# Kernel optimization log

Hardware: AMD Instinct MI355X
Metric: run time of the kernel (lower is better)

Reference implementation:

```python
import jax, jax.numpy as jnp
import numpy as np

N = 100000      # nodes
E = 1600000     # directed edges (avg degree 16)
D_IN, D_H, D_OUT = 128, 128, 64


def glorot(k, fi, fo):
    s = (6.0 / (fi + fo)) ** 0.5
    return jax.random.uniform(k, (fi, fo), jnp.float32, -s, s)


def setup_inputs() -> dict:
    key = jax.random.key(0)
    ks = jax.random.split(key, 5)
    edges = jax.random.randint(ks[0], (2, E), 0, N)
    features = jax.random.normal(ks[1], (N, D_IN), dtype=jnp.float32)
    return dict(
        edges=edges,
        features=features,
        W0=glorot(ks[2], D_IN, D_H), b0=jnp.zeros((D_H,), jnp.float32),
        W1=glorot(ks[3], D_H, D_H), b1=jnp.zeros((D_H,), jnp.float32),
        W2=glorot(ks[4], D_H, D_OUT), b2=jnp.zeros((D_OUT,), jnp.float32),
    )


def _prep(edges):
    # add self-loops and compute symmetric GCN normalization D^-1/2 A_hat D^-1/2
    loop = jnp.arange(N)
    row = jnp.concatenate([edges[0], loop])  # source
    col = jnp.concatenate([edges[1], loop])  # target
    deg = jax.ops.segment_sum(jnp.ones((row.shape[0],), jnp.float32), col, num_segments=N)
    dinv = jnp.where(deg > 0, jax.lax.rsqrt(deg), 0.0)
    norm = dinv[row] * dinv[col]             # per-edge coefficient
    return row, col, norm


def gcn_conv(x, row, col, norm, W, b):
    x = x @ W                                 # [N, out]
    msg = x[row] * norm[:, None]              # gather + scale, [E+N, out]
    return jax.ops.segment_sum(msg, col, num_segments=N) + b


def reference(edges, features, W0, b0, W1, b1, W2, b2):
    row, col, norm = _prep(edges)
    h = jax.nn.relu(gcn_conv(features, row, col, norm, W0, b0))
    h = jax.nn.relu(gcn_conv(h, row, col, norm, W1, b1))
    h = gcn_conv(h, row, col, norm, W2, b2)
    return jax.nn.log_softmax(h, axis=1)
```

## Files before the change

### kernel.cpp

```cpp
#include <hip/hip_runtime.h>
#include <hip/hip_bf16.h>
#include <math.h>

#define NN 100000
#define EE 1600000
#define NB2 391
#define NPART 256
#define STAGE 4864

typedef __attribute__((ext_vector_type(8))) short short8;
typedef __attribute__((ext_vector_type(4))) float f32x4;

__device__ inline unsigned short f2bf(float x) {
    unsigned u = __float_as_uint(x);
    unsigned r = u + 0x7FFFu + ((u >> 16) & 1u);
    return (unsigned short)(r >> 16);
}
__device__ inline unsigned pack2bf(float a, float b) {
    return (unsigned)f2bf(a) | ((unsigned)f2bf(b) << 16);
}
__device__ inline float bflo(unsigned u) { return __uint_as_float(u << 16); }
__device__ inline float bfhi(unsigned u) { return __uint_as_float(u & 0xFFFF0000u); }


__global__ __launch_bounds__(256) void part_hist(const int* __restrict__ dst,
                                                 int* __restrict__ hist, int e) {
    __shared__ int h[NB2];
    for (int i = threadIdx.x; i < NB2; i += 256) h[i] = 0;
    __syncthreads();
    int chunk = (e + NPART - 1) / NPART;
    int b0 = blockIdx.x * chunk, b1 = min(e, b0 + chunk);
    for (int i = b0 + threadIdx.x; i < b1; i += 256)
        atomicAdd(&h[dst[i] >> 8], 1);
    __syncthreads();
    for (int i = threadIdx.x; i < NB2; i += 256)
        hist[i * NPART + blockIdx.x] = h[i];
}

__global__ void scan_block_plain(int* __restrict__ a, int* __restrict__ bsum, int n) {
    __shared__ int s[256];
    int t = threadIdx.x;
    int g = blockIdx.x * 256 + t;
    int v = (g < n) ? a[g] : 0;
    s[t] = v;
    for (int d = 1; d < 256; d <<= 1) {
        __syncthreads();
        int x = (t >= d) ? s[t - d] : 0;
        __syncthreads();
        s[t] += x;
    }
    if (g < n) a[g] = s[t] - v;
    if (t == 255) bsum[blockIdx.x] = s[255];
}

__global__ void scan_sums(int* __restrict__ bsum, int nb) {
    __shared__ int s[512];
    int t = threadIdx.x;
    int v = (t < nb) ? bsum[t] : 0;
    s[t] = v;
    for (int d = 1; d < 512; d <<= 1) {
        __syncthreads();
        int x = (t >= d) ? s[t - d] : 0;
        __syncthreads();
        s[t] += x;
    }
    if (t < nb) bsum[t] = s[t] - v;
}

__global__ void scan_add_plain(int* __restrict__ a, const int* __restrict__ bsum, int n) {
    int g = blockIdx.x * 256 + threadIdx.x;
    if (g < n) a[g] += bsum[blockIdx.x];
}

__global__ __launch_bounds__(256) void part_scatter(const int* __restrict__ src,
                                                    const int* __restrict__ dst,
                                                    const int* __restrict__ hist,
                                                    int2* __restrict__ P, int e) {
    __shared__ int cur[NB2];
    for (int i = threadIdx.x; i < NB2; i += 256) cur[i] = hist[i * NPART + blockIdx.x];
    __syncthreads();
    int chunk = (e + NPART - 1) / NPART;
    int b0 = blockIdx.x * chunk, b1 = min(e, b0 + chunk);
    for (int i = b0 + threadIdx.x; i < b1; i += 256) {
        int d = dst[i];
        int p = atomicAdd(&cur[d >> 8], 1);
        P[p] = make_int2(src[i], d);
    }
}

__global__ __launch_bounds__(256) void bucket_count(const int2* __restrict__ P,
                                                    const int* __restrict__ hist,
                                                    int* __restrict__ offs,
                                                    float* __restrict__ dinv, int e, int n) {
    __shared__ int cnt[256];
    __shared__ int s[256];
    int b = blockIdx.x;
    int t = threadIdx.x;
    int base = hist[b * NPART];
    int end = (b == NB2 - 1) ? e : hist[(b + 1) * NPART];
    cnt[t] = 0;
    __syncthreads();
    for (int i = base + t; i < end; i += 256)
        atomicAdd(&cnt[P[i].y & 255], 1);
    __syncthreads();
    int v = cnt[t];
    s[t] = v;
    for (int d = 1; d < 256; d <<= 1) {
        __syncthreads();
        int x = (t >= d) ? s[t - d] : 0;
        __syncthreads();
        s[t] += x;
    }
    int node = b * 256 + t;
    if (node < n) {
        offs[node] = base + s[t] - v;
        dinv[node] = 1.0f / sqrtf((float)(v + 1));
    }
    if (b == NB2 - 1 && t == 0) offs[n] = e;
}

__global__ __launch_bounds__(256) void bucket_scatter(const int2* __restrict__ P,
                                                      const int* __restrict__ hist,
                                                      const int* __restrict__ offs,
                                                      const float* __restrict__ dinv,
                                                      int2* __restrict__ csr2, int e, int n) {
    __shared__ int cur[256];
    __shared__ int2 stage[STAGE];
    int b = blockIdx.x;
    int t = threadIdx.x;
    int base = hist[b * NPART];
    int end = (b == NB2 - 1) ? e : hist[(b + 1) * NPART];
    int node = b * 256 + t;
    cur[t] = (node < n) ? (offs[node] - base) : 0;
    __syncthreads();
    for (int i = base + t; i < end; i += 256) {
        int2 sd = P[i];
        int p = atomicAdd(&cur[sd.y & 255], 1);
        int2 entry = make_int2(sd.x, __float_as_int(dinv[sd.x]));
        if (p < STAGE) stage[p] = entry;
        else csr2[base + p] = entry;
    }
    __syncthreads();
    int m = end - base;
    if (m > STAGE) m = STAGE;
    for (int i = t; i < m; i += 256) csr2[base + i] = stage[i];
}


__global__ void prep_weights(const float* __restrict__ W0, const float* __restrict__ W1,
                             const float* __restrict__ W2, unsigned short* __restrict__ Wt0,
                             unsigned short* __restrict__ Wt1, unsigned short* __restrict__ Wt2) {
    int g = blockIdx.x * 256 + threadIdx.x;
    if (g < 16384) {
        int n = g >> 7, k = g & 127;
        Wt0[g] = f2bf(W0[k * 128 + n]);
    } else if (g < 32768) {
        int i = g - 16384;
        int n = i >> 7, k = i & 127;
        Wt1[i] = f2bf(W1[k * 128 + n]);
    } else if (g < 40960) {
        int i = g - 32768;
        int n = i >> 7, k = i & 127;
        Wt2[i] = f2bf(W2[k * 64 + n]);
    }
}

template <int DOUT, bool A_IS_F32>
__global__ __launch_bounds__(256) void gemm_mfma(const void* __restrict__ Aptr,
                                                 const unsigned short* __restrict__ Wt,
                                                 unsigned short* __restrict__ Y, int nrows) {
    constexpr int KP = 136;
    constexpr int NT = DOUT / 16;
    __shared__ unsigned short sA[128 * KP];
    __shared__ unsigned short sB[DOUT * KP];
    const int row0 = blockIdx.x * 128;
    const int tid = threadIdx.x;

    for (int i = tid; i < DOUT * 16; i += 256) {
        int n = i >> 4, c = (i & 15) * 8;
        uint4 v = *(const uint4*)(Wt + n * 128 + c);
        *(uint4*)(&sB[n * KP + c]) = v;
    }
    if (A_IS_F32) {
        const float* A = (const float*)Aptr;
        for (int i = tid; i < 128 * 32; i += 256) {
            int r = i >> 5, c = (i & 31) * 4;
            float4 v = make_float4(0.f, 0.f, 0.f, 0.f);
            if (row0 + r < nrows) v = *(const float4*)(A + (size_t)(row0 + r) * 128 + c);
            uint2 o;
            o.x = pack2bf(v.x, v.y);
            o.y = pack2bf(v.z, v.w);
            *(uint2*)(&sA[r * KP + c]) = o;
        }
    } else {
        const unsigned short* A = (const unsigned short*)Aptr;
        for (int i = tid; i < 128 * 16; i += 256) {
            int r = i >> 4, c = (i & 15) * 8;
            uint4 v = make_uint4(0u, 0u, 0u, 0u);
            if (row0 + r < nrows) v = *(const uint4*)(A + (size_t)(row0 + r) * 128 + c);
            *(uint4*)(&sA[r * KP + c]) = v;
        }
    }
    __syncthreads();

    const int wave = tid >> 6;
    const int lane = tid & 63;
    const int m0 = lane & 15;
    const int kq = (lane >> 4) * 8;

    f32x4 acc[2][NT];
#pragma unroll
    for (int rt = 0; rt < 2; ++rt)
#pragma unroll
        for (int t = 0; t < NT; ++t) acc[rt][t] = (f32x4){0.f, 0.f, 0.f, 0.f};

#pragma unroll
    for (int k0 = 0; k0 < 128; k0 += 32) {
        short8 a0 = *(const short8*)(&sA[(wave * 32 + m0) * KP + k0 + kq]);
        short8 a1 = *(const short8*)(&sA[(wave * 32 + 16 + m0) * KP + k0 + kq]);
#pragma unroll
        for (int t = 0; t < NT; ++t) {
            short8 b = *(const short8*)(&sB[(t * 16 + m0) * KP + k0 + kq]);
            acc[0][t] = __builtin_amdgcn_mfma_f32_16x16x32_bf16(a0, b, acc[0][t], 0, 0, 0);
            acc[1][t] = __builtin_amdgcn_mfma_f32_16x16x32_bf16(a1, b, acc[1][t], 0, 0, 0);
        }
    }

#pragma unroll
    for (int rt = 0; rt < 2; ++rt)
#pragma unroll
        for (int t = 0; t < NT; ++t)
#pragma unroll
            for (int r = 0; r < 4; ++r) {
                int row = row0 + wave * 32 + rt * 16 + (lane >> 4) * 4 + r;
                if (row < nrows)
                    Y[(size_t)row * DOUT + t * 16 + (lane & 15)] = f2bf(acc[rt][t][r]);
            }
}

__global__ __launch_bounds__(256) void agg128_bf16(const unsigned short* __restrict__ Xp,
                                                   const int2* __restrict__ csr2,
                                                   const int* __restrict__ offs,
                                                   const float* __restrict__ dinv,
                                                   const float* __restrict__ bias,
                                                   unsigned short* __restrict__ Y, int n) {
    int node = blockIdx.x * 4 + (threadIdx.x >> 6);
    if (node >= n) return;
    int lane = threadIdx.x & 63;
    int q = lane >> 4;
    int l = lane & 15;
    float di = dinv[node];
    int s = offs[node], e = offs[node + 1];
    float a0 = 0.f, a1 = 0.f, a2 = 0.f, a3 = 0.f, a4 = 0.f, a5 = 0.f, a6 = 0.f, a7 = 0.f;
    int p = s + q;
    for (; p + 4 < e; p += 8) {
        int2 sv0 = csr2[p];
        int2 sv1 = csr2[p + 4];
        float c0 = __int_as_float(sv0.y) * di;
        float c1 = __int_as_float(sv1.y) * di;
        uint4 u0 = *(const uint4*)(Xp + (size_t)sv0.x * 128 + l * 8);
        uint4 u1 = *(const uint4*)(Xp + (size_t)sv1.x * 128 + l * 8);
        a0 = fmaf(c0, bflo(u0.x), a0); a1 = fmaf(c0, bfhi(u0.x), a1);
        a2 = fmaf(c0, bflo(u0.y), a2); a3 = fmaf(c0, bfhi(u0.y), a3);
        a4 = fmaf(c0, bflo(u0.z), a4); a5 = fmaf(c0, bfhi(u0.z), a5);
        a6 = fmaf(c0, bflo(u0.w), a6); a7 = fmaf(c0, bfhi(u0.w), a7);
        a0 = fmaf(c1, bflo(u1.x), a0); a1 = fmaf(c1, bfhi(u1.x), a1);
        a2 = fmaf(c1, bflo(u1.y), a2); a3 = fmaf(c1, bfhi(u1.y), a3);
        a4 = fmaf(c1, bflo(u1.z), a4); a5 = fmaf(c1, bfhi(u1.z), a5);
        a6 = fmaf(c1, bflo(u1.w), a6); a7 = fmaf(c1, bfhi(u1.w), a7);
    }
    if (p < e) {
        int2 sv = csr2[p];
        float c = __int_as_float(sv.y) * di;
        uint4 u = *(const uint4*)(Xp + (size_t)sv.x * 128 + l * 8);
        a0 = fmaf(c, bflo(u.x), a0); a1 = fmaf(c, bfhi(u.x), a1);
        a2 = fmaf(c, bflo(u.y), a2); a3 = fmaf(c, bfhi(u.y), a3);
        a4 = fmaf(c, bflo(u.z), a4); a5 = fmaf(c, bfhi(u.z), a5);
        a6 = fmaf(c, bflo(u.w), a6); a7 = fmaf(c, bfhi(u.w), a7);
    }
    if (q == 0) {
        float cs = di * di;
        uint4 u = *(const uint4*)(Xp + (size_t)node * 128 + l * 8);
        a0 = fmaf(cs, bflo(u.x), a0); a1 = fmaf(cs, bfhi(u.x), a1);
        a2 = fmaf(cs, bflo(u.y), a2); a3 = fmaf(cs, bfhi(u.y), a3);
        a4 = fmaf(cs, bflo(u.z), a4); a5 = fmaf(cs, bfhi(u.z), a5);
        a6 = fmaf(cs, bflo(u.w), a6); a7 = fmaf(cs, bfhi(u.w), a7);
    }
    a0 += __shfl_xor(a0, 16); a0 += __shfl_xor(a0, 32);
    a1 += __shfl_xor(a1, 16); a1 += __shfl_xor(a1, 32);
    a2 += __shfl_xor(a2, 16); a2 += __shfl_xor(a2, 32);
    a3 += __shfl_xor(a3, 16); a3 += __shfl_xor(a3, 32);
    a4 += __shfl_xor(a4, 16); a4 += __shfl_xor(a4, 32);
    a5 += __shfl_xor(a5, 16); a5 += __shfl_xor(a5, 32);
    a6 += __shfl_xor(a6, 16); a6 += __shfl_xor(a6, 32);
    a7 += __shfl_xor(a7, 16); a7 += __shfl_xor(a7, 32);
    if (q == 0) {
        float4 bA = *(const float4*)(bias + l * 8);
        float4 bB = *(const float4*)(bias + l * 8 + 4);
        a0 = fmaxf(a0 + bA.x, 0.f); a1 = fmaxf(a1 + bA.y, 0.f);
        a2 = fmaxf(a2 + bA.z, 0.f); a3 = fmaxf(a3 + bA.w, 0.f);
        a4 = fmaxf(a4 + bB.x, 0.f); a5 = fmaxf(a5 + bB.y, 0.f);
        a6 = fmaxf(a6 + bB.z, 0.f); a7 = fmaxf(a7 + bB.w, 0.f);
        uint4 o;
        o.x = pack2bf(a0, a1); o.y = pack2bf(a2, a3);
        o.z = pack2bf(a4, a5); o.w = pack2bf(a6, a7);
        *(uint4*)(Y + (size_t)node * 128 + l * 8) = o;
    }
}

__global__ __launch_bounds__(256) void agg_softmax64_bf16(const unsigned short* __restrict__ Xp,
                                                          const int2* __restrict__ csr2,
                                                          const int* __restrict__ offs,
                                                          const float* __restrict__ dinv,
                                                          const float* __restrict__ bias,
                                                          float* __restrict__ out, int n) {
    int node = blockIdx.x * 4 + (threadIdx.x >> 6);
    if (node >= n) return;
    int lane = threadIdx.x & 63;
    int g8 = lane >> 3;
    int l = lane & 7;
    float di = dinv[node];
    int s = offs[node], e = offs[node + 1];
    float a0 = 0.f, a1 = 0.f, a2 = 0.f, a3 = 0.f, a4 = 0.f, a5 = 0.f, a6 = 0.f, a7 = 0.f;
    int p = s + g8;
    for (; p + 8 < e; p += 16) {
        int2 sv0 = csr2[p];
        int2 sv1 = csr2[p + 8];
        float c0 = __int_as_float(sv0.y) * di;
        float c1 = __int_as_float(sv1.y) * di;
        uint4 u0 = *(const uint4*)(Xp + (size_t)sv0.x * 64 + l * 8);
        uint4 u1 = *(const uint4*)(Xp + (size_t)sv1.x * 64 + l * 8);
        a0 = fmaf(c0, bflo(u0.x), a0); a1 = fmaf(c0, bfhi(u0.x), a1);
        a2 = fmaf(c0, bflo(u0.y), a2); a3 = fmaf(c0, bfhi(u0.y), a3);
        a4 = fmaf(c0, bflo(u0.z), a4); a5 = fmaf(c0, bfhi(u0.z), a5);
        a6 = fmaf(c0, bflo(u0.w), a6); a7 = fmaf(c0, bfhi(u0.w), a7);
        a0 = fmaf(c1, bflo(u1.x), a0); a1 = fmaf(c1, bfhi(u1.x), a1);
        a2 = fmaf(c1, bflo(u1.y), a2); a3 = fmaf(c1, bfhi(u1.y), a3);
        a4 = fmaf(c1, bflo(u1.z), a4); a5 = fmaf(c1, bfhi(u1.z), a5);
        a6 = fmaf(c1, bflo(u1.w), a6); a7 = fmaf(c1, bfhi(u1.w), a7);
    }
    if (p < e) {
        int2 sv = csr2[p];
        float c = __int_as_float(sv.y) * di;
        uint4 u = *(const uint4*)(Xp + (size_t)sv.x * 64 + l * 8);
        a0 = fmaf(c, bflo(u.x), a0); a1 = fmaf(c, bfhi(u.x), a1);
        a2 = fmaf(c, bflo(u.y), a2); a3 = fmaf(c, bfhi(u.y), a3);
        a4 = fmaf(c, bflo(u.z), a4); a5 = fmaf(c, bfhi(u.z), a5);
        a6 = fmaf(c, bflo(u.w), a6); a7 = fmaf(c, bfhi(u.w), a7);
    }
    if (g8 == 0) {
        float cs = di * di;
        uint4 u = *(const uint4*)(Xp + (size_t)node * 64 + l * 8);
        a0 = fmaf(cs, bflo(u.x), a0); a1 = fmaf(cs, bfhi(u.x), a1);
        a2 = fmaf(cs, bflo(u.y), a2); a3 = fmaf(cs, bfhi(u.y), a3);
        a4 = fmaf(cs, bflo(u.z), a4); a5 = fmaf(cs, bfhi(u.z), a5);
        a6 = fmaf(cs, bflo(u.w), a6); a7 = fmaf(cs, bfhi(u.w), a7);
    }
    a0 += __shfl_xor(a0, 8); a0 += __shfl_xor(a0, 16); a0 += __shfl_xor(a0, 32);
    a1 += __shfl_xor(a1, 8); a1 += __shfl_xor(a1, 16); a1 += __shfl_xor(a1, 32);
    a2 += __shfl_xor(a2, 8); a2 += __shfl_xor(a2, 16); a2 += __shfl_xor(a2, 32);
    a3 += __shfl_xor(a3, 8); a3 += __shfl_xor(a3, 16); a3 += __shfl_xor(a3, 32);
    a4 += __shfl_xor(a4, 8); a4 += __shfl_xor(a4, 16); a4 += __shfl_xor(a4, 32);
    a5 += __shfl_xor(a5, 8); a5 += __shfl_xor(a5, 16); a5 += __shfl_xor(a5, 32);
    a6 += __shfl_xor(a6, 8); a6 += __shfl_xor(a6, 16); a6 += __shfl_xor(a6, 32);
    a7 += __shfl_xor(a7, 8); a7 += __shfl_xor(a7, 16); a7 += __shfl_xor(a7, 32);
    if (g8 == 0) {
        float4 bA = *(const float4*)(bias + l * 8);
        float4 bB = *(const float4*)(bias + l * 8 + 4);
        a0 += bA.x; a1 += bA.y; a2 += bA.z; a3 += bA.w;
        a4 += bB.x; a5 += bB.y; a6 += bB.z; a7 += bB.w;
        float m = fmaxf(fmaxf(fmaxf(a0, a1), fmaxf(a2, a3)), fmaxf(fmaxf(a4, a5), fmaxf(a6, a7)));
#pragma unroll
        for (int o = 4; o > 0; o >>= 1) m = fmaxf(m, __shfl_xor(m, o));
        float ssum = __expf(a0 - m) + __expf(a1 - m) + __expf(a2 - m) + __expf(a3 - m) +
                     __expf(a4 - m) + __expf(a5 - m) + __expf(a6 - m) + __expf(a7 - m);
#pragma unroll
        for (int o = 4; o > 0; o >>= 1) ssum += __shfl_xor(ssum, o);
        float lg = m + __logf(ssum);
        float4 r0 = make_float4(a0 - lg, a1 - lg, a2 - lg, a3 - lg);
        float4 r1 = make_float4(a4 - lg, a5 - lg, a6 - lg, a7 - lg);
        *(float4*)(out + (size_t)node * 64 + l * 8) = r0;
        *(float4*)(out + (size_t)node * 64 + l * 8 + 4) = r1;
    }
}


extern "C" void kernel_launch(void* const* d_in, const int* in_sizes, int n_in,
                              void* d_out, int out_size, void* d_ws, size_t ws_size,
                              hipStream_t stream) {
    const int* edges = (const int*)d_in[0];
    const float* feat = (const float*)d_in[1];
    const float* W0 = (const float*)d_in[2];
    const float* b0 = (const float*)d_in[3];
    const float* W1 = (const float*)d_in[4];
    const float* b1 = (const float*)d_in[5];
    const float* W2 = (const float*)d_in[6];
    const float* b2 = (const float*)d_in[7];

    const int N = NN;
    const int E = EE;
    const int HN = NB2 * NPART;
    const int HB = HN / 256;

    char* ws = (char*)d_ws;
    int* hist = (int*)ws;
    int* bsum = hist + HN;
    int* offs = bsum + 512;
    float* dinv = (float*)(offs + N + 1);
    size_t io = (size_t)((char*)(dinv + N) - ws);
    io = (io + 15) & ~(size_t)15;
    int2* P = (int2*)(ws + io);
    int2* csr2 = P + E;
    unsigned short* Wt0 = (unsigned short*)(csr2 + E);
    unsigned short* Wt1 = Wt0 + 16384;
    unsigned short* Wt2 = Wt1 + 16384;
    size_t off = (size_t)((char*)(Wt2 + 8192) - ws);
    off = (off + 255) & ~(size_t)255;
    unsigned short* bufA = (unsigned short*)(ws + off);
    unsigned short* bufB = bufA + (size_t)N * 128;

    const int* esrc = edges;
    const int* edst = edges + E;

    prep_weights<<<160, 256, 0, stream>>>(W0, W1, W2, Wt0, Wt1, Wt2);
    part_hist<<<NPART, 256, 0, stream>>>(edst, hist, E);
    scan_block_plain<<<HB, 256, 0, stream>>>(hist, bsum, HN);
    scan_sums<<<1, 512, 0, stream>>>(bsum, HB);
    scan_add_plain<<<HB, 256, 0, stream>>>(hist, bsum, HN);
    part_scatter<<<NPART, 256, 0, stream>>>(esrc, edst, hist, P, E);
    bucket_count<<<NB2, 256, 0, stream>>>(P, hist, offs, dinv, E, N);
    bucket_scatter<<<NB2, 256, 0, stream>>>(P, hist, offs, dinv, csr2, E, N);

    const int gemmBlocks = (N + 127) / 128;
    const int aggBlocks = (N + 3) / 4;

    gemm_mfma<128, true><<<gemmBlocks, 256, 0, stream>>>(feat, Wt0, bufA, N);
    agg128_bf16<<<aggBlocks, 256, 0, stream>>>(bufA, csr2, offs, dinv, b0, bufB, N);
    gemm_mfma<128, false><<<gemmBlocks, 256, 0, stream>>>(bufB, Wt1, bufA, N);
    agg128_bf16<<<aggBlocks, 256, 0, stream>>>(bufA, csr2, offs, dinv, b1, bufB, N);
    gemm_mfma<64, false><<<gemmBlocks, 256, 0, stream>>>(bufB, Wt2, bufA, N);
    agg_softmax64_bf16<<<aggBlocks, 256, 0, stream>>>(bufA, csr2, offs, dinv, b2, (float*)d_out, N);
}
```

Baseline: 419.2 us.

## Fold source-side normalization into GEMM epilogue and shrink CSR to plain indices

Each GEMM output row is now pre-scaled by dinv[row], so aggregation sums neighbor rows without per-edge coefficients and applies the destination dinv once at the end. The CSR entries drop from (src, dinv) int2 pairs to a single int, and partition entries pack src and the low destination bits into one int. The two bucket kernels merge into a single kernel. The 128-wide aggregation loop is unrolled to four outstanding gathers. These changes cut edge-stream bytes and per-edge multiplies in the memory-bound gather. The cost is one extra bf16 rounding of pre-scaled values, and the packing assumes src << 8 fits in 31 bits.

```diff
diff --git a/kernel.cpp b/kernel.cpp
--- a/kernel.cpp
+++ b/kernel.cpp
@@ -6,10 +6,11 @@
 #define EE 1600000
 #define NB2 391
 #define NPART 256
-#define STAGE 4864
+#define STAGE 6144
 
 typedef __attribute__((ext_vector_type(8))) short short8;
 typedef __attribute__((ext_vector_type(4))) float f32x4;
+typedef __attribute__((ext_vector_type(2))) float f32x2;
 
 __device__ inline unsigned short f2bf(float x) {
     unsigned u = __float_as_uint(x);
@@ -19,8 +20,12 @@
 __device__ inline unsigned pack2bf(float a, float b) {
     return (unsigned)f2bf(a) | ((unsigned)f2bf(b) << 16);
 }
-__device__ inline float bflo(unsigned u) { return __uint_as_float(u << 16); }
-__device__ inline float bfhi(unsigned u) { return __uint_as_float(u & 0xFFFF0000u); }
+__device__ inline f32x2 bf2f2(unsigned u) {
+    f32x2 r;
+    r.x = __uint_as_float(u << 16);
+    r.y = __uint_as_float(u & 0xFFFF0000u);
+    return r;
+}
 
 
 __global__ __launch_bounds__(256) void part_hist(const int* __restrict__ dst,
@@ -75,7 +80,7 @@
 __global__ __launch_bounds__(256) void part_scatter(const int* __restrict__ src,
                                                     const int* __restrict__ dst,
                                                     const int* __restrict__ hist,
-                                                    int2* __restrict__ P, int e) {
+                                                    int* __restrict__ P, int e) {
     __shared__ int cur[NB2];
     for (int i = threadIdx.x; i < NB2; i += 256) cur[i] = hist[i * NPART + blockIdx.x];
     __syncthreads();
@@ -84,66 +89,56 @@
     for (int i = b0 + threadIdx.x; i < b1; i += 256) {
         int d = dst[i];
         int p = atomicAdd(&cur[d >> 8], 1);
-        P[p] = make_int2(src[i], d);
-    }
-}
-
-__global__ __launch_bounds__(256) void bucket_count(const int2* __restrict__ P,
+        P[p] = (src[i] << 8) | (d & 255);
+    }
+}
+
+__global__ __launch_bounds__(256) void bucket_build(const int* __restrict__ P,
                                                     const int* __restrict__ hist,
                                                     int* __restrict__ offs,
-                                                    float* __restrict__ dinv, int e, int n) {
+                                                    float* __restrict__ dinv,
+                                                    int* __restrict__ csr, int e, int n) {
     __shared__ int cnt[256];
-    __shared__ int s[256];
-    int b = blockIdx.x;
-    int t = threadIdx.x;
+    __shared__ int sc[256];
+    __shared__ int cur[256];
+    __shared__ int stage[STAGE];
+    int b = blockIdx.x, t = threadIdx.x;
     int base = hist[b * NPART];
     int end = (b == NB2 - 1) ? e : hist[(b + 1) * NPART];
     cnt[t] = 0;
     __syncthreads();
     for (int i = base + t; i < end; i += 256)
-        atomicAdd(&cnt[P[i].y & 255], 1);
+        atomicAdd(&cnt[P[i] & 255], 1);
     __syncthreads();
     int v = cnt[t];
-    s[t] = v;
+    sc[t] = v;
     for (int d = 1; d < 256; d <<= 1) {
         __syncthreads();
-        int x = (t >= d) ? s[t - d] : 0;
-        __syncthreads();
-        s[t] += x;
-    }
+        int x = (t >= d) ? sc[t - d] : 0;
+        __syncthreads();
+        sc[t] += x;
+    }
+    __syncthreads();
+    int myoff = sc[t] - v;
     int node = b * 256 + t;
     if (node < n) {
-        offs[node] = base + s[t] - v;
+        offs[node] = base + myoff;
         dinv[node] = 1.0f / sqrtf((float)(v + 1));
     }
     if (b == NB2 - 1 && t == 0) offs[n] = e;
-}
-
-__global__ __launch_bounds__(256) void bucket_scatter(const int2* __restrict__ P,
-                                                      const int* __restrict__ hist,
-                                                      const int* __restrict__ offs,
-                                                      const float* __restrict__ dinv,
-                                                      int2* __restrict__ csr2, int e, int n) {
-    __shared__ int cur[256];
-    __shared__ int2 stage[STAGE];
-    int b = blockIdx.x;
-    int t = threadIdx.x;
-    int base = hist[b * NPART];
-    int end = (b == NB2 - 1) ? e : hist[(b + 1) * NPART];
-    int node = b * 256 + t;
-    cur[t] = (node < n) ? (offs[node] - base) : 0;
+    cur[t] = myoff;
     __syncthreads();
     for (int i = base + t; i < end; i += 256) {
-        int2 sd = P[i];
-        int p = atomicAdd(&cur[sd.y & 255], 1);
-        int2 entry = make_int2(sd.x, __float_as_int(dinv[sd.x]));
-        if (p < STAGE) stage[p] = entry;
-        else csr2[base + p] = entry;
+        int pe = P[i];
+        int p = atomicAdd(&cur[pe & 255], 1);
+        int sv = ((unsigned)pe) >> 8;
+        if (p < STAGE) stage[p] = sv;
+        else csr[base + p] = sv;
     }
     __syncthreads();
     int m = end - base;
     if (m > STAGE) m = STAGE;
-    for (int i = t; i < m; i += 256) csr2[base + i] = stage[i];
+    for (int i = t; i < m; i += 256) csr[base + i] = stage[i];
 }
 
 
@@ -168,6 +163,7 @@
 template <int DOUT, bool A_IS_F32>
 __global__ __launch_bounds__(256) void gemm_mfma(const void* __restrict__ Aptr,
                                                  const unsigned short* __restrict__ Wt,
+                                                 const float* __restrict__ dinv,
                                                  unsigned short* __restrict__ Y, int nrows) {
     constexpr int KP = 136;
     constexpr int NT = DOUT / 16;
@@ -229,17 +225,19 @@
 #pragma unroll
     for (int rt = 0; rt < 2; ++rt)
 #pragma unroll
-        for (int t = 0; t < NT; ++t)
-#pragma unroll
-            for (int r = 0; r < 4; ++r) {
-                int row = row0 + wave * 32 + rt * 16 + (lane >> 4) * 4 + r;
-                if (row < nrows)
-                    Y[(size_t)row * DOUT + t * 16 + (lane & 15)] = f2bf(acc[rt][t][r]);
+        for (int r = 0; r < 4; ++r) {
+            int row = row0 + wave * 32 + rt * 16 + (lane >> 4) * 4 + r;
+            if (row < nrows) {
+                float dv = dinv[row];
+#pragma unroll
+                for (int t = 0; t < NT; ++t)
+                    Y[(size_t)row * DOUT + t * 16 + (lane & 15)] = f2bf(acc[rt][t][r] * dv);
             }
+        }
 }
 
 __global__ __launch_bounds__(256) void agg128_bf16(const unsigned short* __restrict__ Xp,
-                                                   const int2* __restrict__ csr2,
+                                                   const int* __restrict__ csr,
                                                    const int* __restrict__ offs,
                                                    const float* __restrict__ dinv,
                                                    const float* __restrict__ bias,
@@ -249,67 +247,56 @@
     int lane = threadIdx.x & 63;
     int q = lane >> 4;
     int l = lane & 15;
-    float di = dinv[node];
     int s = offs[node], e = offs[node + 1];
-    float a0 = 0.f, a1 = 0.f, a2 = 0.f, a3 = 0.f, a4 = 0.f, a5 = 0.f, a6 = 0.f, a7 = 0.f;
+    f32x2 a0 = {0.f, 0.f}, a1 = {0.f, 0.f}, a2 = {0.f, 0.f}, a3 = {0.f, 0.f};
     int p = s + q;
-    for (; p + 4 < e; p += 8) {
-        int2 sv0 = csr2[p];
-        int2 sv1 = csr2[p + 4];
-        float c0 = __int_as_float(sv0.y) * di;
-        float c1 = __int_as_float(sv1.y) * di;
-        uint4 u0 = *(const uint4*)(Xp + (size_t)sv0.x * 128 + l * 8);
-        uint4 u1 = *(const uint4*)(Xp + (size_t)sv1.x * 128 + l * 8);
-        a0 = fmaf(c0, bflo(u0.x), a0); a1 = fmaf(c0, bfhi(u0.x), a1);
-        a2 = fmaf(c0, bflo(u0.y), a2); a3 = fmaf(c0, bfhi(u0.y), a3);
-        a4 = fmaf(c0, bflo(u0.z), a4); a5 = fmaf(c0, bfhi(u0.z), a5);
-        a6 = fmaf(c0, bflo(u0.w), a6); a7 = fmaf(c0, bfhi(u0.w), a7);
-        a0 = fmaf(c1, bflo(u1.x), a0); a1 = fmaf(c1, bfhi(u1.x), a1);
-        a2 = fmaf(c1, bflo(u1.y), a2); a3 = fmaf(c1, bfhi(u1.y), a3);
-        a4 = fmaf(c1, bflo(u1.z), a4); a5 = fmaf(c1, bfhi(u1.z), a5);
-        a6 = fmaf(c1, bflo(u1.w), a6); a7 = fmaf(c1, bfhi(u1.w), a7);
-    }
-    if (p < e) {
-        int2 sv = csr2[p];
-        float c = __int_as_float(sv.y) * di;
-        uint4 u = *(const uint4*)(Xp + (size_t)sv.x * 128 + l * 8);
-        a0 = fmaf(c, bflo(u.x), a0); a1 = fmaf(c, bfhi(u.x), a1);
-        a2 = fmaf(c, bflo(u.y), a2); a3 = fmaf(c, bfhi(u.y), a3);
-        a4 = fmaf(c, bflo(u.z), a4); a5 = fmaf(c, bfhi(u.z), a5);
-        a6 = fmaf(c, bflo(u.w), a6); a7 = fmaf(c, bfhi(u.w), a7);
+    for (; p + 12 < e; p += 16) {
+        int s0 = csr[p], s1 = csr[p + 4], s2 = csr[p + 8], s3 = csr[p + 12];
+        uint4 u0 = *(const uint4*)(Xp + (size_t)s0 * 128 + l * 8);
+        uint4 u1 = *(const uint4*)(Xp + (size_t)s1 * 128 + l * 8);
+        uint4 u2 = *(const uint4*)(Xp + (size_t)s2 * 128 + l * 8);
+        uint4 u3 = *(const uint4*)(Xp + (size_t)s3 * 128 + l * 8);
+        a0 += bf2f2(u0.x); a1 += bf2f2(u0.y); a2 += bf2f2(u0.z); a3 += bf2f2(u0.w);
+        a0 += bf2f2(u1.x); a1 += bf2f2(u1.y); a2 += bf2f2(u1.z); a3 += bf2f2(u1.w);
+        a0 += bf2f2(u2.x); a1 += bf2f2(u2.y); a2 += bf2f2(u2.z); a3 += bf2f2(u2.w);
+        a0 += bf2f2(u3.x); a1 += bf2f2(u3.y); a2 += bf2f2(u3.z); a3 += bf2f2(u3.w);
+    }
+    for (; p < e; p += 4) {
+        int s0 = csr[p];
+        uint4 u = *(const uint4*)(Xp + (size_t)s0 * 128 + l * 8);
+        a0 += bf2f2(u.x); a1 += bf2f2(u.y); a2 += bf2f2(u.z); a3 += bf2f2(u.w);
     }
     if (q == 0) {
-        float cs = di * di;
         uint4 u = *(const uint4*)(Xp + (size_t)node * 128 + l * 8);
-        a0 = fmaf(cs, bflo(u.x), a0); a1 = fmaf(cs, bfhi(u.x), a1);
-        a2 = fmaf(cs, bflo(u.y), a2); a3 = fmaf(cs, bfhi(u.y), a3);
-        a4 = fmaf(cs, bflo(u.z), a4); a5 = fmaf(cs, bfhi(u.z), a5);
-        a6 = fmaf(cs, bflo(u.w), a6); a7 = fmaf(cs, bfhi(u.w), a7);
-    }
-    a0 += __shfl_xor(a0, 16); a0 += __shfl_xor(a0, 32);
-    a1 += __shfl_xor(a1, 16); a1 += __shfl_xor(a1, 32);
-    a2 += __shfl_xor(a2, 16); a2 += __shfl_xor(a2, 32);
-    a3 += __shfl_xor(a3, 16); a3 += __shfl_xor(a3, 32);
-    a4 += __shfl_xor(a4, 16); a4 += __shfl_xor(a4, 32);
-    a5 += __shfl_xor(a5, 16); a5 += __shfl_xor(a5, 32);
-    a6 += __shfl_xor(a6, 16); a6 += __shfl_xor(a6, 32);
-    a7 += __shfl_xor(a7, 16); a7 += __shfl_xor(a7, 32);
+        a0 += bf2f2(u.x); a1 += bf2f2(u.y); a2 += bf2f2(u.z); a3 += bf2f2(u.w);
+    }
+    float r0 = a0.x, r1 = a0.y, r2 = a1.x, r3 = a1.y;
+    float r4 = a2.x, r5 = a2.y, r6 = a3.x, r7 = a3.y;
+    r0 += __shfl_xor(r0, 16); r0 += __shfl_xor(r0, 32);
+    r1 += __shfl_xor(r1, 16); r1 += __shfl_xor(r1, 32);
+    r2 += __shfl_xor(r2, 16); r2 += __shfl_xor(r2, 32);
+    r3 += __shfl_xor(r3, 16); r3 += __shfl_xor(r3, 32);
+    r4 += __shfl_xor(r4, 16); r4 += __shfl_xor(r4, 32);
+    r5 += __shfl_xor(r5, 16); r5 += __shfl_xor(r5, 32);
+    r6 += __shfl_xor(r6, 16); r6 += __shfl_xor(r6, 32);
+    r7 += __shfl_xor(r7, 16); r7 += __shfl_xor(r7, 32);
     if (q == 0) {
+        float di = dinv[node];
         float4 bA = *(const float4*)(bias + l * 8);
         float4 bB = *(const float4*)(bias + l * 8 + 4);
-        a0 = fmaxf(a0 + bA.x, 0.f); a1 = fmaxf(a1 + bA.y, 0.f);
-        a2 = fmaxf(a2 + bA.z, 0.f); a3 = fmaxf(a3 + bA.w, 0.f);
-        a4 = fmaxf(a4 + bB.x, 0.f); a5 = fmaxf(a5 + bB.y, 0.f);
-        a6 = fmaxf(a6 + bB.z, 0.f); a7 = fmaxf(a7 + bB.w, 0.f);
+        r0 = fmaxf(fmaf(di, r0, bA.x), 0.f); r1 = fmaxf(fmaf(di, r1, bA.y), 0.f);
+        r2 = fmaxf(fmaf(di, r2, bA.z), 0.f); r3 = fmaxf(fmaf(di, r3, bA.w), 0.f);
+        r4 = fmaxf(fmaf(di, r4, bB.x), 0.f); r5 = fmaxf(fmaf(di, r5, bB.y), 0.f);
+        r6 = fmaxf(fmaf(di, r6, bB.z), 0.f); r7 = fmaxf(fmaf(di, r7, bB.w), 0.f);
         uint4 o;
-        o.x = pack2bf(a0, a1); o.y = pack2bf(a2, a3);
-        o.z = pack2bf(a4, a5); o.w = pack2bf(a6, a7);
+        o.x = pack2bf(r0, r1); o.y = pack2bf(r2, r3);
+        o.z = pack2bf(r4, r5); o.w = pack2bf(r6, r7);
         *(uint4*)(Y + (size_t)node * 128 + l * 8) = o;
     }
 }
 
 __global__ __launch_bounds__(256) void agg_softmax64_bf16(const unsigned short* __restrict__ Xp,
-                                                          const int2* __restrict__ csr2,
+                                                          const int* __restrict__ csr,
                                                           const int* __restrict__ offs,
                                                           const float* __restrict__ dinv,
                                                           const float* __restrict__ bias,
@@ -319,68 +306,55 @@
     int lane = threadIdx.x & 63;
     int g8 = lane >> 3;
     int l = lane & 7;
-    float di = dinv[node];
     int s = offs[node], e = offs[node + 1];
-    float a0 = 0.f, a1 = 0.f, a2 = 0.f, a3 = 0.f, a4 = 0.f, a5 = 0.f, a6 = 0.f, a7 = 0.f;
+    f32x2 a0 = {0.f, 0.f}, a1 = {0.f, 0.f}, a2 = {0.f, 0.f}, a3 = {0.f, 0.f};
     int p = s + g8;
     for (; p + 8 < e; p += 16) {
-        int2 sv0 = csr2[p];
-        int2 sv1 = csr2[p + 8];
-        float c0 = __int_as_float(sv0.y) * di;
-        float c1 = __int_as_float(sv1.y) * di;
-        uint4 u0 = *(const uint4*)(Xp + (size_t)sv0.x * 64 + l * 8);
-        uint4 u1 = *(const uint4*)(Xp + (size_t)sv1.x * 64 + l * 8);
-        a0 = fmaf(c0, bflo(u0.x), a0); a1 = fmaf(c0, bfhi(u0.x), a1);
-        a2 = fmaf(c0, bflo(u0.y), a2); a3 = fmaf(c0, bfhi(u0.y), a3);
-        a4 = fmaf(c0, bflo(u0.z), a4); a5 = fmaf(c0, bfhi(u0.z), a5);
-        a6 = fmaf(c0, bflo(u0.w), a6); a7 = fmaf(c0, bfhi(u0.w), a7);
-        a0 = fmaf(c1, bflo(u1.x), a0); a1 = fmaf(c1, bfhi(u1.x), a1);
-        a2 = fmaf(c1, bflo(u1.y), a2); a3 = fmaf(c1, bfhi(u1.y), a3);
-        a4 = fmaf(c1, bflo(u1.z), a4); a5 = fmaf(c1, bfhi(u1.z), a5);
-        a6 = fmaf(c1, bflo(u1.w), a6); a7 = fmaf(c1, bfhi(u1.w), a7);
+        int s0 = csr[p], s1 = csr[p + 8];
+        uint4 u0 = *(const uint4*)(Xp + (size_t)s0 * 64 + l * 8);
+        uint4 u1 = *(const uint4*)(Xp + (size_t)s1 * 64 + l * 8);
+        a0 += bf2f2(u0.x); a1 += bf2f2(u0.y); a2 += bf2f2(u0.z); a3 += bf2f2(u0.w);
+        a0 += bf2f2(u1.x); a1 += bf2f2(u1.y); a2 += bf2f2(u1.z); a3 += bf2f2(u1.w);
     }
     if (p < e) {
-        int2 sv = csr2[p];
-        float c = __int_as_float(sv.y) * di;
-        uint4 u = *(const uint4*)(Xp + (size_t)sv.x * 64 + l * 8);
-        a0 = fmaf(c, bflo(u.x), a0); a1 = fmaf(c, bfhi(u.x), a1);
-        a2 = fmaf(c, bflo(u.y), a2); a3 = fmaf(c, bfhi(u.y), a3);
-        a4 = fmaf(c, bflo(u.z), a4); a5 = fmaf(c, bfhi(u.z), a5);
-        a6 = fmaf(c, bflo(u.w), a6); a7 = fmaf(c, bfhi(u.w), a7);
+        int s0 = csr[p];
+        uint4 u = *(const uint4*)(Xp + (size_t)s0 * 64 + l * 8);
+        a0 += bf2f2(u.x); a1 += bf2f2(u.y); a2 += bf2f2(u.z); a3 += bf2f2(u.w);
     }
     if (g8 == 0) {
-        float cs = di * di;
         uint4 u = *(const uint4*)(Xp + (size_t)node * 64 + l * 8);
-        a0 = fmaf(cs, bflo(u.x), a0); a1 = fmaf(cs, bfhi(u.x), a1);
-        a2 = fmaf(cs, bflo(u.y), a2); a3 = fmaf(cs, bfhi(u.y), a3);
-        a4 = fmaf(cs, bflo(u.z), a4); a5 = fmaf(cs, bfhi(u.z), a5);
-        a6 = fmaf(cs, bflo(u.w), a6); a7 = fmaf(cs, bfhi(u.w), a7);
-    }
-    a0 += __shfl_xor(a0, 8); a0 += __shfl_xor(a0, 16); a0 += __shfl_xor(a0, 32);
-    a1 += __shfl_xor(a1, 8); a1 += __shfl_xor(a1, 16); a1 += __shfl_xor(a1, 32);
-    a2 += __shfl_xor(a2, 8); a2 += __shfl_xor(a2, 16); a2 += __shfl_xor(a2, 32);
-    a3 += __shfl_xor(a3, 8); a3 += __shfl_xor(a3, 16); a3 += __shfl_xor(a3, 32);
-    a4 += __shfl_xor(a4, 8); a4 += __shfl_xor(a4, 16); a4 += __shfl_xor(a4, 32);
-    a5 += __shfl_xor(a5, 8); a5 += __shfl_xor(a5, 16); a5 += __shfl_xor(a5, 32);
-    a6 += __shfl_xor(a6, 8); a6 += __shfl_xor(a6, 16); a6 += __shfl_xor(a6, 32);
-    a7 += __shfl_xor(a7, 8); a7 += __shfl_xor(a7, 16); a7 += __shfl_xor(a7, 32);
+        a0 += bf2f2(u.x); a1 += bf2f2(u.y); a2 += bf2f2(u.z); a3 += bf2f2(u.w);
+    }
+    float r0 = a0.x, r1 = a0.y, r2 = a1.x, r3 = a1.y;
+    float r4 = a2.x, r5 = a2.y, r6 = a3.x, r7 = a3.y;
+    r0 += __shfl_xor(r0, 8); r0 += __shfl_xor(r0, 16); r0 += __shfl_xor(r0, 32);
+    r1 += __shfl_xor(r1, 8); r1 += __shfl_xor(r1, 16); r1 += __shfl_xor(r1, 32);
+    r2 += __shfl_xor(r2, 8); r2 += __shfl_xor(r2, 16); r2 += __shfl_xor(r2, 32);
+    r3 += __shfl_xor(r3, 8); r3 += __shfl_xor(r3, 16); r3 += __shfl_xor(r3, 32);
+    r4 += __shfl_xor(r4, 8); r4 += __shfl_xor(r4, 16); r4 += __shfl_xor(r4, 32);
+    r5 += __shfl_xor(r5, 8); r5 += __shfl_xor(r5, 16); r5 += __shfl_xor(r5, 32);
+    r6 += __shfl_xor(r6, 8); r6 += __shfl_xor(r6, 16); r6 += __shfl_xor(r6, 32);
+    r7 += __shfl_xor(r7, 8); r7 += __shfl_xor(r7, 16); r7 += __shfl_xor(r7, 32);
     if (g8 == 0) {
+        float di = dinv[node];
         float4 bA = *(const float4*)(bias + l * 8);
         float4 bB = *(const float4*)(bias + l * 8 + 4);
-        a0 += bA.x; a1 += bA.y; a2 += bA.z; a3 += bA.w;
-        a4 += bB.x; a5 += bB.y; a6 += bB.z; a7 += bB.w;
-        float m = fmaxf(fmaxf(fmaxf(a0, a1), fmaxf(a2, a3)), fmaxf(fmaxf(a4, a5), fmaxf(a6, a7)));
+        r0 = fmaf(di, r0, bA.x); r1 = fmaf(di, r1, bA.y);
+        r2 = fmaf(di, r2, bA.z); r3 = fmaf(di, r3, bA.w);
+        r4 = fmaf(di, r4, bB.x); r5 = fmaf(di, r5, bB.y);
+        r6 = fmaf(di, r6, bB.z); r7 = fmaf(di, r7, bB.w);
+        float m = fmaxf(fmaxf(fmaxf(r0, r1), fmaxf(r2, r3)), fmaxf(fmaxf(r4, r5), fmaxf(r6, r7)));
 #pragma unroll
         for (int o = 4; o > 0; o >>= 1) m = fmaxf(m, __shfl_xor(m, o));
-        float ssum = __expf(a0 - m) + __expf(a1 - m) + __expf(a2 - m) + __expf(a3 - m) +
-                     __expf(a4 - m) + __expf(a5 - m) + __expf(a6 - m) + __expf(a7 - m);
+        float ssum = __expf(r0 - m) + __expf(r1 - m) + __expf(r2 - m) + __expf(r3 - m) +
+                     __expf(r4 - m) + __expf(r5 - m) + __expf(r6 - m) + __expf(r7 - m);
 #pragma unroll
         for (int o = 4; o > 0; o >>= 1) ssum += __shfl_xor(ssum, o);
         float lg = m + __logf(ssum);
-        float4 r0 = make_float4(a0 - lg, a1 - lg, a2 - lg, a3 - lg);
-        float4 r1 = make_float4(a4 - lg, a5 - lg, a6 - lg, a7 - lg);
-        *(float4*)(out + (size_t)node * 64 + l * 8) = r0;
-        *(float4*)(out + (size_t)node * 64 + l * 8 + 4) = r1;
+        float4 o0 = make_float4(r0 - lg, r1 - lg, r2 - lg, r3 - lg);
+        float4 o1 = make_float4(r4 - lg, r5 - lg, r6 - lg, r7 - lg);
+        *(float4*)(out + (size_t)node * 64 + l * 8) = o0;
+        *(float4*)(out + (size_t)node * 64 + l * 8 + 4) = o1;
     }
 }
 
@@ -407,11 +381,9 @@
     int* bsum = hist + HN;
     int* offs = bsum + 512;
     float* dinv = (float*)(offs + N + 1);
-    size_t io = (size_t)((char*)(dinv + N) - ws);
-    io = (io + 15) & ~(size_t)15;
-    int2* P = (int2*)(ws + io);
-    int2* csr2 = P + E;
-    unsigned short* Wt0 = (unsigned short*)(csr2 + E);
+    int* P = (int*)(dinv + N);
+    int* csr = P + E;
+    unsigned short* Wt0 = (unsigned short*)(csr + E);
     unsigned short* Wt1 = Wt0 + 16384;
     unsigned short* Wt2 = Wt1 + 16384;
     size_t off = (size_t)((char*)(Wt2 + 8192) - ws);
@@ -428,16 +400,15 @@
     scan_sums<<<1, 512, 0, stream>>>(bsum, HB);
     scan_add_plain<<<HB, 256, 0, stream>>>(hist, bsum, HN);
     part_scatter<<<NPART, 256, 0, stream>>>(esrc, edst, hist, P, E);
-    bucket_count<<<NB2, 256, 0, stream>>>(P, hist, offs, dinv, E, N);
-    bucket_scatter<<<NB2, 256, 0, stream>>>(P, hist, offs, dinv, csr2, E, N);
+    bucket_build<<<NB2, 256, 0, stream>>>(P, hist, offs, dinv, csr, E, N);
 
     const int gemmBlocks = (N + 127) / 128;
     const int aggBlocks = (N + 3) / 4;
 
-    gemm_mfma<128, true><<<gemmBlocks, 256, 0, stream>>>(feat, Wt0, bufA, N);
-    agg128_bf16<<<aggBlocks, 256, 0, stream>>>(bufA, csr2, offs, dinv, b0, bufB, N);
-    gemm_mfma<128, false><<<gemmBlocks, 256, 0, stream>>>(bufB, Wt1, bufA, N);
-    agg128_bf16<<<aggBlocks, 256, 0, stream>>>(bufA, csr2, offs, dinv, b1, bufB, N);
-    gemm_mfma<64, false><<<gemmBlocks, 256, 0, stream>>>(bufB, Wt2, bufA, N);
-    agg_softmax64_bf16<<<aggBlocks, 256, 0, stream>>>(bufA, csr2, offs, dinv, b2, (float*)d_out, N);
-}
+    gemm_mfma<128, true><<<gemmBlocks, 256, 0, stream>>>(feat, Wt0, dinv, bufA, N);
+    agg128_bf16<<<aggBlocks, 256, 0, stream>>>(bufA, csr, offs, dinv, b0, bufB, N);
+    gemm_mfma<128, false><<<gemmBlocks, 256, 0, stream>>>(bufB, Wt1, dinv, bufA, N);
+    agg128_bf16<<<aggBlocks, 256, 0, stream>>>(bufA, csr, offs, dinv, b1, bufB, N);
+    gemm_mfma<64, false><<<gemmBlocks, 256, 0, stream>>>(bufB, Wt2, dinv, bufA, N);
+    agg_softmax64_bf16<<<aggBlocks, 256, 0, stream>>>(bufA, csr, offs, dinv, b2, (float*)d_out, N);
+}
```

After: 409.1 us. 2.4% less time.
